# Performance work log

Hardware: AMD Instinct MI355X
Metric: run time of the kernel (lower is better)

The kernel has to match this reference:

```python
import jax, jax.numpy as jnp
import numpy as np

B, T, D = 128, 256, 1024   # batch, input_steps, input_dim
H, V, S = 1024, 1024, 128  # hidden_dim, output_dim, output_seq_length


def setup_inputs() -> dict:
    key = jax.random.key(0)
    ks = jax.random.split(key, 16)
    def w(k, shape, fan_in):
        bound = 1.0 / np.sqrt(fan_in)
        return jax.random.uniform(k, shape, jnp.float32, -bound, bound)
    return {
        "h": jax.random.normal(ks[0], (B, T, D), jnp.float32),
        # linear_h_a: Linear(D, H, bias=False); torch weight is (out, in)
        "w_h_a": w(ks[1], (H, D), D),
        # linear_s_a: Linear(H, H, bias=True)
        "w_s_a": w(ks[2], (H, H), H),
        "b_s_a": w(ks[3], (H,), H),
        # linear_a: Linear(H, 1, bias=False)
        "w_a": w(ks[4], (1, H), H),
        # linear_init_s: Linear(D, H, bias=True)
        "w_init_s": w(ks[5], (H, D), D),
        "b_init_s": w(ks[6], (H,), D),
        # GRUCell(V + D, H)
        "gru_w_ih": w(ks[7], (3 * H, V + D), H),
        "gru_w_hh": w(ks[8], (3 * H, H), H),
        "gru_b_ih": w(ks[9], (3 * H,), H),
        "gru_b_hh": w(ks[10], (3 * H,), H),
        # RNNCell(H + D, V), tanh nonlinearity
        "rnn_w_ih": w(ks[11], (V, H + D), V),
        "rnn_w_hh": w(ks[12], (V, V), V),
        "rnn_b_ih": w(ks[13], (V,), V),
        "rnn_b_hh": w(ks[14], (V,), V),
    }


def reference(h, w_h_a, w_s_a, b_s_a, w_a, w_init_s, b_init_s,
              gru_w_ih, gru_w_hh, gru_b_ih, gru_b_hh,
              rnn_w_ih, rnn_w_hh, rnn_b_ih, rnn_b_hh):
    wh = jnp.einsum('btd,hd->bth', h, w_h_a)                 # precomputed W_h @ h
    s0 = jnp.tanh(h[:, 0, :] @ w_init_s.T + b_init_s)        # (B, H)
    y0 = jnp.zeros((h.shape[0], rnn_w_ih.shape[0]), h.dtype)  # (B, V)

    def step(carry, _):
        s, y = carry
        # additive (Bahdanau) attention scores over input steps
        e = jnp.tanh(wh + (s @ w_s_a.T + b_s_a)[:, None, :])  # (B, T, H)
        scores = jnp.einsum('bth,h->bt', e, w_a[0])           # (B, T)
        a = jax.nn.softmax(scores, axis=1)
        c = jnp.einsum('bt,btd->bd', a, h)                    # context (B, D)
        # GRUCell: input = [c, y_prev], hidden = s
        x = jnp.concatenate([c, y], axis=1)
        gi = x @ gru_w_ih.T + gru_b_ih
        gh = s @ gru_w_hh.T + gru_b_hh
        ir, iz, inn = jnp.split(gi, 3, axis=1)
        hr, hz, hn = jnp.split(gh, 3, axis=1)
        r = jax.nn.sigmoid(ir + hr)
        z = jax.nn.sigmoid(iz + hz)
        n = jnp.tanh(inn + r * hn)
        s_new = (1.0 - z) * n + z * s
        # RNNCell(tanh): input = [c, s_new], hidden = y_prev; then softmax
        xr = jnp.concatenate([c, s_new], axis=1)
        pre = xr @ rnn_w_ih.T + rnn_b_ih + y @ rnn_w_hh.T + rnn_b_hh
        y_new = jax.nn.softmax(jnp.tanh(pre), axis=1)
        return (s_new, y_new), y_new

    _, ys = jax.lax.scan(step, (s0, y0), None, length=S)      # ys: (S, B, V)
    return jnp.transpose(ys, (1, 0, 2))                       # (B, S, V)
```

## Files before the change

### kernel.cpp

```cpp
#include <hip/hip_runtime.h>

typedef __bf16 bf16;
typedef __bf16 v8bf __attribute__((ext_vector_type(8)));
typedef __bf16 v4bf __attribute__((ext_vector_type(4)));
typedef float  v4f  __attribute__((ext_vector_type(4)));


static __device__ __forceinline__ float fast_tanh(float x) {
  x = fminf(fmaxf(x, -10.f), 10.f);
  float e = __expf(2.f * x);
  return (e - 1.f) * __builtin_amdgcn_rcpf(e + 1.f);
}
static __device__ __forceinline__ float fast_sigmoid(float x) {
  return __builtin_amdgcn_rcpf(1.f + __expf(-x));
}

static __device__ __forceinline__ size_t packOff(int r, int k) {
  return ((size_t)((r >> 4) * 32 + (k >> 5)) * 64 + ((k >> 3) & 3) * 16 + (r & 15)) * 8 + (k & 7);
}

template<int NKS>
static __device__ __forceinline__ void gemmTile(const bf16* __restrict__ Ap,
                                                const bf16* __restrict__ Bp,
                                                int m0, int n0, int ks0,
                                                v4f acc[2][2]) {
  const int lane = threadIdx.x & 63;
  const int w = threadIdx.x >> 6;
  const int wr = w >> 1, wc = w & 1;
  const bf16* a0p = Ap + (((size_t)((m0 >> 4) + wr * 2) * 32 + ks0) * 64 + lane) * 8;
  const bf16* b0p = Bp + (((size_t)((n0 >> 4) + wc * 2) * 32 + ks0) * 64 + lane) * 8;
#pragma unroll 8
  for (int ks = 0; ks < NKS; ks++) {
    v8bf a0 = *(const v8bf*)(a0p);
    v8bf a1 = *(const v8bf*)(a0p + 16384);
    v8bf b0 = *(const v8bf*)(b0p);
    v8bf b1 = *(const v8bf*)(b0p + 16384);
    a0p += 512; b0p += 512;
    acc[0][0] = __builtin_amdgcn_mfma_f32_16x16x32_bf16(a0, b0, acc[0][0], 0, 0, 0);
    acc[0][1] = __builtin_amdgcn_mfma_f32_16x16x32_bf16(a0, b1, acc[0][1], 0, 0, 0);
    acc[1][0] = __builtin_amdgcn_mfma_f32_16x16x32_bf16(a1, b0, acc[1][0], 0, 0, 0);
    acc[1][1] = __builtin_amdgcn_mfma_f32_16x16x32_bf16(a1, b1, acc[1][1], 0, 0, 0);
  }
}

static __device__ __forceinline__ void storeTileF32(float* __restrict__ C, int ldc,
                                                    int m0, int n0, v4f acc[2][2]) {
  const int lane = threadIdx.x & 63, w = threadIdx.x >> 6;
  const int wr = w >> 1, wc = w & 1;
  const int mB = m0 + wr * 32 + (lane >> 4) * 4;
  const int nB = n0 + wc * 32 + (lane & 15);
#pragma unroll
  for (int mf = 0; mf < 2; mf++)
#pragma unroll
    for (int nf = 0; nf < 2; nf++)
#pragma unroll
      for (int i = 0; i < 4; i++)
        C[(size_t)(mB + mf * 16 + i) * ldc + nB + nf * 16] = acc[mf][nf][i];
}

__global__ __launch_bounds__(256) void kPack(const float* __restrict__ src, int ld,
                                             bf16* __restrict__ dst, int nTh) {
  int th = blockIdx.x * 256 + threadIdx.x;
  if (th >= nTh) return;
  int rb = th >> 11, ks = (th >> 6) & 31, l = th & 63;
  int r = rb * 16 + (l & 15);
  int k = ks * 32 + ((l >> 4) & 3) * 8;
  const float* s = src + (size_t)r * ld + k;
  v4f v0 = *(const v4f*)(s);
  v4f v1 = *(const v4f*)(s + 4);
  v8bf o;
#pragma unroll
  for (int e = 0; e < 4; e++) { o[e] = (bf16)v0[e]; o[4 + e] = (bf16)v1[e]; }
  *(v8bf*)(dst + (size_t)th * 8) = o;
}

__global__ __launch_bounds__(256) void kCast4(const float* __restrict__ src,
                                              bf16* __restrict__ dst, int n4) {
  int i = blockIdx.x * 256 + threadIdx.x;
  if (i < n4) {
    v4f v = ((const v4f*)src)[i];
    ((v4bf*)dst)[i] = __builtin_convertvector(v, v4bf);
  }
}

__global__ __launch_bounds__(256) void kPrep(const float* rnn_b_ih, const float* rnn_b_hh,
                                             float* bsum, bf16* y_b16p) {
  int th = blockIdx.x * 256 + threadIdx.x;
  if (th < 16384) {
    v8bf z = {};
    ((v8bf*)y_b16p)[th] = z;
  } else {
    int j = th - 16384;
    bsum[j] = rnn_b_ih[j] + rnn_b_hh[j];
  }
}

__global__ __launch_bounds__(256) void kGemmTW(const bf16* __restrict__ Ap,
                                               const bf16* __restrict__ Bp,
                                               bf16* __restrict__ C) {
  const int nt = blockIdx.x & 15, mt = blockIdx.x >> 4;
  v4f acc[2][2] = {};
  gemmTile<32>(Ap, Bp, mt * 64, nt * 64, 0, acc);
  const int lane = threadIdx.x & 63, w = threadIdx.x >> 6;
  const int wr = w >> 1, wc = w & 1;
  const int mB = mt * 64 + wr * 32 + (lane >> 4) * 4;
  const int nB = nt * 64 + wc * 32 + (lane & 15);
#pragma unroll
  for (int mf = 0; mf < 2; mf++)
#pragma unroll
    for (int nf = 0; nf < 2; nf++)
#pragma unroll
      for (int i = 0; i < 4; i++)
        C[(size_t)(mB + mf * 16 + i) * 1024 + nB + nf * 16] = (bf16)fast_tanh(acc[mf][nf][i]);
}

__global__ __launch_bounds__(256) void kGemmS0(const bf16* __restrict__ Ap,
                                               const bf16* __restrict__ Bp,
                                               const float* __restrict__ bias,
                                               float* __restrict__ sF, bf16* __restrict__ sB) {
  const int nt = blockIdx.x & 15, mt = blockIdx.x >> 4;
  v4f acc[2][2] = {};
  gemmTile<32>(Ap, Bp, mt * 64, nt * 64, 0, acc);
  const int lane = threadIdx.x & 63, w = threadIdx.x >> 6;
  const int wr = w >> 1, wc = w & 1;
  const int mB = mt * 64 + wr * 32 + (lane >> 4) * 4;
  const int nB = nt * 64 + wc * 32 + (lane & 15);
#pragma unroll
  for (int mf = 0; mf < 2; mf++)
#pragma unroll
    for (int nf = 0; nf < 2; nf++) {
      const int n = nB + nf * 16;
      float bv = bias[n];
#pragma unroll
      for (int i = 0; i < 4; i++) {
        const int m = mB + mf * 16 + i;
        float v = fast_tanh(acc[mf][nf][i] + bv);
        size_t pi = packOff(m, n);
        sF[pi] = v;
        sB[pi] = (bf16)v;
      }
    }
}

__global__ __launch_bounds__(256) void kGemmPS(const bf16* __restrict__ Ap,
                                               const bf16* __restrict__ Bp,
                                               float* __restrict__ PS0, float* __restrict__ PS1) {
  const int t = blockIdx.x;
  const int kh = t & 1, mh = (t >> 1) & 1, nt = t >> 2;
  v4f acc[2][2] = {};
  gemmTile<16>(Ap, Bp, mh * 64, nt * 64, kh * 16, acc);
  storeTileF32(kh ? PS1 : PS0, 5120, mh * 64, nt * 64, acc);
}


static __device__ __forceinline__ void outPhase(
    int b, int step,
    const float* __restrict__ PS0, const float* __restrict__ PS1,
    const float* __restrict__ gcp0, const float* __restrict__ gcp1,
    const float* __restrict__ ygp, const float* __restrict__ bsum,
    float* __restrict__ out, bf16* __restrict__ y_b16p, float* smred) {
  const int tid = threadIdx.x, lane = tid & 63, w = tid >> 6;
  const int v0 = tid * 4;
  const size_t o5 = (size_t)b * 5120 + v0;
  const size_t o4 = (size_t)b * 4096 + 3072 + v0;
  v4f pre = *(const v4f*)(PS0 + o5);
  pre += *(const v4f*)(PS1 + o5);
  pre += *(const v4f*)(gcp0 + o4);
  pre += *(const v4f*)(gcp1 + o4);
  pre += *(const v4f*)(ygp + o4);
  pre += *(const v4f*)(bsum + v0);
  float ee[4];
  float psum = 0.f;
#pragma unroll
  for (int i = 0; i < 4; i++) { ee[i] = __expf(fast_tanh(pre[i])); psum += ee[i]; }
#pragma unroll
  for (int off = 32; off; off >>= 1) psum += __shfl_down(psum, off, 64);
  if (lane == 0) smred[w] = psum;
  __syncthreads();
  const float rden = __builtin_amdgcn_rcpf(smred[0] + smred[1] + smred[2] + smred[3]);
  v4f y4;
#pragma unroll
  for (int i = 0; i < 4; i++) y4[i] = ee[i] * rden;
  *(v4f*)(out + ((size_t)b * 128 + step) * 1024 + v0) = y4;
  *(v4bf*)(y_b16p + packOff(b, v0)) = __builtin_convertvector(y4, v4bf);
}

__global__ __launch_bounds__(256) void kScoresOut(
    const float* __restrict__ PS0, const float* __restrict__ PS1,
    const float* __restrict__ b_s_a, const float* __restrict__ w_a,
    const bf16* __restrict__ twb,
    const float* __restrict__ gcp0, const float* __restrict__ gcp1,
    const float* __restrict__ ygp, const float* __restrict__ bsum,
    float* __restrict__ esh_g, float* __restrict__ out,
    bf16* __restrict__ y_b16p, int step) {
  __shared__ float sm[2052];
  const int tid = threadIdx.x, lane = tid & 63, w = tid >> 6;
  if (blockIdx.x >= 256) {
    if (step == 0) return;
    outPhase(blockIdx.x - 256, step - 1, PS0, PS1, gcp0, gcp1, ygp, bsum,
             out, y_b16p, sm + 2048);
    return;
  }
  const int b = blockIdx.x >> 1, half = blockIdx.x & 1;
  float* ts = sm;
  float* wa = sm + 1024;
#pragma unroll
  for (int jj = 0; jj < 4; jj++) {
    int j = tid + jj * 256;
    float sa = PS0[(size_t)b * 5120 + 1024 + j] + PS1[(size_t)b * 5120 + 1024 + j] + b_s_a[j];
    float t = fast_tanh(sa);
    ts[j] = fminf(fmaxf(t, -0.99999994f), 0.99999994f);
    wa[j] = w_a[j];
  }
  __syncthreads();
  float tj[16], wj[16];
  const int h0 = lane * 16;
#pragma unroll
  for (int j = 0; j < 16; j++) { tj[j] = ts[h0 + j]; wj[j] = wa[h0 + j]; }
  const bf16* twB = twb + ((size_t)b * 256 + half * 128 + w * 32) * 1024 + h0;
  for (int ti = 0; ti < 32; ti++) {
    const bf16* p = twB + (size_t)ti * 1024;
    v8bf t8a = *(const v8bf*)p;
    v8bf t8b = *(const v8bf*)(p + 8);
    float acc = 0.f;
#pragma unroll
    for (int j = 0; j < 8; j++) {
      float tv = (float)t8a[j];
      acc += wj[j] * (tv + tj[j]) * __builtin_amdgcn_rcpf(__builtin_fmaf(tv, tj[j], 1.f));
      float tv2 = (float)t8b[j];
      acc += wj[8 + j] * (tv2 + tj[8 + j]) * __builtin_amdgcn_rcpf(__builtin_fmaf(tv2, tj[8 + j], 1.f));
    }
#pragma unroll
    for (int off = 32; off; off >>= 1) acc += __shfl_down(acc, off, 64);
    if (lane == 0) esh_g[(size_t)b * 256 + half * 128 + w * 32 + ti] = __expf(acc);
  }
}

__global__ __launch_bounds__(256) void kCtxY(
    const float* __restrict__ esh_g, const bf16* __restrict__ hb,
    const bf16* __restrict__ y_b16p, const bf16* __restrict__ W2p,
    bf16* __restrict__ c_b16p, float* __restrict__ ygp) {
  __shared__ float sm[1028];
  const int tid = threadIdx.x, lane = tid & 63, w = tid >> 6;
  if (blockIdx.x < 128) {
    const int b = blockIdx.x;
    float ev = esh_g[(size_t)b * 256 + tid];
    sm[tid] = ev;
    float p = ev;
#pragma unroll
    for (int off = 32; off; off >>= 1) p += __shfl_down(p, off, 64);
    if (lane == 0) sm[1024 + w] = p;
    __syncthreads();
    const float rden = __builtin_amdgcn_rcpf(sm[1024] + sm[1025] + sm[1026] + sm[1027]);
    const int d0 = tid * 4;
    const bf16* hp = hb + (size_t)b * 262144 + d0;
    v4f cacc = {};
#pragma unroll 8
    for (int t = 0; t < 256; t++) {
      v4bf h4 = *(const v4bf*)hp;
      hp += 1024;
      cacc += sm[t] * __builtin_convertvector(h4, v4f);
    }
    cacc *= rden;
    *(v4bf*)(c_b16p + packOff(b, d0)) = __builtin_convertvector(cacc, v4bf);
  } else {
    const int tile = blockIdx.x - 128;
    const int nt = tile & 63, mh = tile >> 6;
    v4f acc[2][2] = {};
    gemmTile<32>(y_b16p, W2p, mh * 64, nt * 64, 0, acc);
    storeTileF32(ygp, 4096, mh * 64, nt * 64, acc);
  }
}

__global__ __launch_bounds__(256) void kCGemm(
    const bf16* __restrict__ c_b16p, const bf16* __restrict__ W3p,
    float* __restrict__ gcp0, float* __restrict__ gcp1) {
  const int kh = blockIdx.x & 1, mh = (blockIdx.x >> 1) & 1, nt = blockIdx.x >> 2;
  v4f acc[2][2] = {};
  gemmTile<16>(c_b16p, W3p, mh * 64, nt * 64, kh * 16, acc);
  storeTileF32(kh ? gcp1 : gcp0, 4096, mh * 64, nt * 64, acc);
}

__global__ __launch_bounds__(256) void kGru(
    const float* __restrict__ gcp0, const float* __restrict__ gcp1,
    const float* __restrict__ ygp,
    const float* __restrict__ PS0, const float* __restrict__ PS1,
    const float* __restrict__ gru_b_ih, const float* __restrict__ gru_b_hh,
    float* __restrict__ s_f32p, bf16* __restrict__ s_b16p) {
  const int th = blockIdx.x * 256 + threadIdx.x;
  const int rb = th >> 11, ks = (th >> 6) & 31, l = th & 63;
  const int r = rb * 16 + (l & 15);
  const int j0 = ks * 32 + ((l >> 4) & 3) * 8;
  const float* g0 = gcp0 + (size_t)r * 4096 + j0;
  const float* g1 = gcp1 + (size_t)r * 4096 + j0;
  const float* yg = ygp + (size_t)r * 4096 + j0;
  const float* p0 = PS0 + (size_t)r * 5120 + j0;
  const float* p1 = PS1 + (size_t)r * 5120 + j0;
  const float* bih = gru_b_ih + j0;
  const float* bhh = gru_b_hh + j0;
  float sv[8], sn[8];
  *(v4f*)sv = *(const v4f*)(s_f32p + (size_t)th * 8);
  *(v4f*)(sv + 4) = *(const v4f*)(s_f32p + (size_t)th * 8 + 4);
#pragma unroll
  for (int e = 0; e < 8; e++) {
    float ir  = g0[e] + g1[e] + yg[e] + bih[e];
    float iz  = g0[1024 + e] + g1[1024 + e] + yg[1024 + e] + bih[1024 + e];
    float in_ = g0[2048 + e] + g1[2048 + e] + yg[2048 + e] + bih[2048 + e];
    float hr = p0[2048 + e] + p1[2048 + e] + bhh[e];
    float hz = p0[3072 + e] + p1[3072 + e] + bhh[1024 + e];
    float hn = p0[4096 + e] + p1[4096 + e] + bhh[2048 + e];
    float rg = fast_sigmoid(ir + hr);
    float zg = fast_sigmoid(iz + hz);
    float ng = fast_tanh(in_ + rg * hn);
    sn[e] = (1.f - zg) * ng + zg * sv[e];
  }
  *(v4f*)(s_f32p + (size_t)th * 8) = *(v4f*)sn;
  *(v4f*)(s_f32p + (size_t)th * 8 + 4) = *(v4f*)(sn + 4);
  v8bf sb;
#pragma unroll
  for (int e = 0; e < 8; e++) sb[e] = (bf16)sn[e];
  *(v8bf*)(s_b16p + (size_t)th * 8) = sb;
}

__global__ __launch_bounds__(256) void kOutFinal(
    const float* __restrict__ PS0, const float* __restrict__ PS1,
    const float* __restrict__ gcp0, const float* __restrict__ gcp1,
    const float* __restrict__ ygp, const float* __restrict__ bsum,
    float* __restrict__ out, bf16* __restrict__ y_b16p) {
  __shared__ float smred[4];
  outPhase(blockIdx.x, 127, PS0, PS1, gcp0, gcp1, ygp, bsum, out, y_b16p, smred);
}

extern "C" void kernel_launch(void* const* d_in, const int* in_sizes, int n_in,
                              void* d_out, int out_size, void* d_ws, size_t ws_size,
                              hipStream_t stream) {
  const float* h        = (const float*)d_in[0];
  const float* w_h_a    = (const float*)d_in[1];
  const float* w_s_a    = (const float*)d_in[2];
  const float* b_s_a    = (const float*)d_in[3];
  const float* w_a      = (const float*)d_in[4];
  const float* w_init_s = (const float*)d_in[5];
  const float* b_init_s = (const float*)d_in[6];
  const float* gru_w_ih = (const float*)d_in[7];
  const float* gru_w_hh = (const float*)d_in[8];
  const float* gru_b_ih = (const float*)d_in[9];
  const float* gru_b_hh = (const float*)d_in[10];
  const float* rnn_w_ih = (const float*)d_in[11];
  const float* rnn_w_hh = (const float*)d_in[12];
  const float* rnn_b_ih = (const float*)d_in[13];
  const float* rnn_b_hh = (const float*)d_in[14];
  (void)in_sizes; (void)n_in; (void)out_size; (void)ws_size;

  char* p = (char*)d_ws;
  auto alloc = [&](size_t bytes) { char* r = p; p += (bytes + 255) & ~(size_t)255; return r; };
  bf16* hbig   = (bf16*)alloc(33554432ull * 2);
  bf16* twb    = (bf16*)alloc(33554432ull * 2);
  bf16* h0p    = (bf16*)alloc(131072ull * 2);
  bf16* wbha_p = (bf16*)alloc(1048576ull * 2);
  bf16* wbini_p= (bf16*)alloc(1048576ull * 2);
  bf16* W2p    = (bf16*)alloc(4194304ull * 2);
  bf16* W3p    = (bf16*)alloc(4194304ull * 2);
  bf16* WP5p   = (bf16*)alloc(5242880ull * 2);
  float* PS0   = (float*)alloc(128ull * 5120 * 4);
  float* PS1   = (float*)alloc(128ull * 5120 * 4);
  float* gcp0  = (float*)alloc(128ull * 4096 * 4);
  float* gcp1  = (float*)alloc(128ull * 4096 * 4);
  float* ygp   = (float*)alloc(128ull * 4096 * 4);
  float* esh_g = (float*)alloc(128ull * 256 * 4);
  float* s_f32p= (float*)alloc(131072ull * 4);
  float* bsum  = (float*)alloc(1024ull * 4);
  bf16* s_b16p = (bf16*)alloc(131072ull * 2);
  bf16* y_b16p = (bf16*)alloc(131072ull * 2);
  bf16* c_b16p = (bf16*)alloc(131072ull * 2);
  float* out = (float*)d_out;

  kPack<<<dim3(16384), 256, 0, stream>>>(h, 1024, hbig, 4194304);
  kPack<<<dim3(64),    256, 0, stream>>>(h, 262144, h0p, 16384);
  kPack<<<dim3(512),   256, 0, stream>>>(w_h_a, 1024, wbha_p, 131072);
  kPack<<<dim3(512),   256, 0, stream>>>(w_init_s, 1024, wbini_p, 131072);
  kPack<<<dim3(1536),  256, 0, stream>>>(gru_w_ih, 2048, W3p, 393216);
  kPack<<<dim3(512),   256, 0, stream>>>(rnn_w_ih, 2048, W3p + 3145728, 131072);
  kPack<<<dim3(1536),  256, 0, stream>>>(gru_w_ih + 1024, 2048, W2p, 393216);
  kPack<<<dim3(512),   256, 0, stream>>>(rnn_w_hh, 1024, W2p + 3145728, 131072);
  kPack<<<dim3(512),   256, 0, stream>>>(rnn_w_ih + 1024, 2048, WP5p, 131072);
  kPack<<<dim3(512),   256, 0, stream>>>(w_s_a, 1024, WP5p + 1048576, 131072);
  kPack<<<dim3(1536),  256, 0, stream>>>(gru_w_hh, 1024, WP5p + 2097152, 393216);
  kPrep<<<dim3(68), 256, 0, stream>>>(rnn_b_ih, rnn_b_hh, bsum, y_b16p);

  kGemmTW<<<dim3(8192), 256, 0, stream>>>(hbig, wbha_p, twb);
  kCast4<<<dim3(32768), 256, 0, stream>>>(h, hbig, 8388608);
  kGemmS0<<<dim3(32), 256, 0, stream>>>(h0p, wbini_p, b_init_s, s_f32p, s_b16p);
  kGemmPS<<<dim3(320), 256, 0, stream>>>(s_b16p, WP5p, PS0, PS1);

  for (int step = 0; step < 128; step++) {
    kScoresOut<<<dim3(384), 256, 0, stream>>>(PS0, PS1, b_s_a, w_a, twb,
                                              gcp0, gcp1, ygp, bsum,
                                              esh_g, out, y_b16p, step);
    kCtxY<<<dim3(256), 256, 0, stream>>>(esh_g, hbig, y_b16p, W2p, c_b16p, ygp);
    kCGemm<<<dim3(256), 256, 0, stream>>>(c_b16p, W3p, gcp0, gcp1);
    kGru<<<dim3(64), 256, 0, stream>>>(gcp0, gcp1, ygp, PS0, PS1,
                                       gru_b_ih, gru_b_hh, s_f32p, s_b16p);
    kGemmPS<<<dim3(320), 256, 0, stream>>>(s_b16p, WP5p, PS0, PS1);
  }
  kOutFinal<<<dim3(128), 256, 0, stream>>>(PS0, PS1, gcp0, gcp1, ygp, bsum, out, y_b16p);
}
```

Measured before the change: 8.712 ms.

## Fuse per-step kernels into scores+context and a combined X-GEMM+GRU kernel

Cuts the per-step kernel chain from five launches to three. Attention scores and the unnormalized context are fused into one kernel, with softmax normalization deferred via partial sums. The context and y GEMMs are merged into a single concatenated-input GEMM whose epilogue applies the GRU update and emits the RNN pre-activation. The tanh-based score is also rewritten algebraically using exp(2x) precomputation, which is meant to remove per-element tanh and the extra passes through global memory. In exchange, the new exponential form risks overflow or precision loss in bf16.

```diff
diff --git a/kernel.cpp b/kernel.cpp
--- a/kernel.cpp
+++ b/kernel.cpp
@@ -15,11 +15,11 @@
   return __builtin_amdgcn_rcpf(1.f + __expf(-x));
 }
 
-static __device__ __forceinline__ size_t packOff(int r, int k) {
-  return ((size_t)((r >> 4) * 32 + (k >> 5)) * 64 + ((k >> 3) & 3) * 16 + (r & 15)) * 8 + (k & 7);
-}
-
-template<int NKS>
+static __device__ __forceinline__ size_t packOffN(int r, int k, int nksb) {
+  return ((size_t)((r >> 4) * nksb + (k >> 5)) * 64 + ((k >> 3) & 3) * 16 + (r & 15)) * 8 + (k & 7);
+}
+
+template<int NKS, int NKSB>
 static __device__ __forceinline__ void gemmTile(const bf16* __restrict__ Ap,
                                                 const bf16* __restrict__ Bp,
                                                 int m0, int n0, int ks0,
@@ -27,14 +27,14 @@
   const int lane = threadIdx.x & 63;
   const int w = threadIdx.x >> 6;
   const int wr = w >> 1, wc = w & 1;
-  const bf16* a0p = Ap + (((size_t)((m0 >> 4) + wr * 2) * 32 + ks0) * 64 + lane) * 8;
-  const bf16* b0p = Bp + (((size_t)((n0 >> 4) + wc * 2) * 32 + ks0) * 64 + lane) * 8;
+  const bf16* a0p = Ap + (((size_t)((m0 >> 4) + wr * 2) * NKSB + ks0) * 64 + lane) * 8;
+  const bf16* b0p = Bp + (((size_t)((n0 >> 4) + wc * 2) * NKSB + ks0) * 64 + lane) * 8;
 #pragma unroll 8
   for (int ks = 0; ks < NKS; ks++) {
     v8bf a0 = *(const v8bf*)(a0p);
-    v8bf a1 = *(const v8bf*)(a0p + 16384);
+    v8bf a1 = *(const v8bf*)(a0p + NKSB * 512);
     v8bf b0 = *(const v8bf*)(b0p);
-    v8bf b1 = *(const v8bf*)(b0p + 16384);
+    v8bf b1 = *(const v8bf*)(b0p + NKSB * 512);
     a0p += 512; b0p += 512;
     acc[0][0] = __builtin_amdgcn_mfma_f32_16x16x32_bf16(a0, b0, acc[0][0], 0, 0, 0);
     acc[0][1] = __builtin_amdgcn_mfma_f32_16x16x32_bf16(a0, b1, acc[0][1], 0, 0, 0);
@@ -58,8 +58,8 @@
         C[(size_t)(mB + mf * 16 + i) * ldc + nB + nf * 16] = acc[mf][nf][i];
 }
 
-__global__ __launch_bounds__(256) void kPack(const float* __restrict__ src, int ld,
-                                             bf16* __restrict__ dst, int nTh) {
+__global__ __launch_bounds__(256) void kPackG(const float* __restrict__ src, int ld,
+                                              bf16* __restrict__ dst, int nTh, int r0) {
   int th = blockIdx.x * 256 + threadIdx.x;
   if (th >= nTh) return;
   int rb = th >> 11, ks = (th >> 6) & 31, l = th & 63;
@@ -71,6 +71,30 @@
   v8bf o;
 #pragma unroll
   for (int e = 0; e < 4; e++) { o[e] = (bf16)v0[e]; o[4 + e] = (bf16)v1[e]; }
+  *(v8bf*)(dst + packOffN(r0 + r, k, 32)) = o;
+}
+
+__global__ __launch_bounds__(256) void kPackW(const float* __restrict__ gih,
+                                              const float* __restrict__ rih,
+                                              const float* __restrict__ rhh,
+                                              bf16* __restrict__ dst) {
+  const int th = blockIdx.x * 256 + threadIdx.x;
+  const int rb = th >> 12;
+  const int ks = (th >> 6) & 63;
+  const int l = th & 63;
+  const int n = rb * 16 + (l & 15);
+  const int k = ks * 32 + ((l >> 4) & 3) * 8;
+  const int g = (n >> 4) & 3;
+  const int j = ((n >> 6) << 4) | (n & 15);
+  const float* s;
+  if (g < 3)            s = gih + (size_t)(g * 1024 + j) * 2048 + k;
+  else if (k < 1024)    s = rih + (size_t)j * 2048 + k;
+  else                  s = rhh + (size_t)j * 1024 + (k - 1024);
+  v4f v0 = *(const v4f*)(s);
+  v4f v1 = *(const v4f*)(s + 4);
+  v8bf o;
+#pragma unroll
+  for (int e = 0; e < 4; e++) { o[e] = (bf16)v0[e]; o[4 + e] = (bf16)v1[e]; }
   *(v8bf*)(dst + (size_t)th * 8) = o;
 }
 
@@ -83,24 +107,38 @@
   }
 }
 
-__global__ __launch_bounds__(256) void kPrep(const float* rnn_b_ih, const float* rnn_b_hh,
-                                             float* bsum, bf16* y_b16p) {
-  int th = blockIdx.x * 256 + threadIdx.x;
-  if (th < 16384) {
+__global__ __launch_bounds__(256) void kPrep(const float* __restrict__ rnn_b_ih,
+                                             const float* __restrict__ rnn_b_hh,
+                                             const float* __restrict__ w_a,
+                                             float* __restrict__ bsum,
+                                             float* __restrict__ wsum,
+                                             bf16* __restrict__ xcatp) {
+  __shared__ float sred[4];
+  if (blockIdx.x < 64) {
+    int th = blockIdx.x * 256 + threadIdx.x;
+    int rb = th >> 11, ks = 64 + ((th >> 6) & 31), l = th & 63;
     v8bf z = {};
-    ((v8bf*)y_b16p)[th] = z;
+    *(v8bf*)(xcatp + ((size_t)(rb * 96 + ks) * 64 + l) * 8) = z;
   } else {
-    int j = th - 16384;
-    bsum[j] = rnn_b_ih[j] + rnn_b_hh[j];
-  }
-}
-
-__global__ __launch_bounds__(256) void kGemmTW(const bf16* __restrict__ Ap,
-                                               const bf16* __restrict__ Bp,
-                                               bf16* __restrict__ C) {
+    int t = threadIdx.x;
+    v4f a = *(const v4f*)(rnn_b_ih + t * 4);
+    v4f c = *(const v4f*)(rnn_b_hh + t * 4);
+    *(v4f*)(bsum + t * 4) = a + c;
+    float zz = w_a[t] + w_a[256 + t] + w_a[512 + t] + w_a[768 + t];
+#pragma unroll
+    for (int off = 32; off; off >>= 1) zz += __shfl_down(zz, off, 64);
+    if ((t & 63) == 0) sred[t >> 6] = zz;
+    __syncthreads();
+    if (t == 0) wsum[0] = sred[0] + sred[1] + sred[2] + sred[3];
+  }
+}
+
+__global__ __launch_bounds__(256) void kGemmE(const bf16* __restrict__ Ap,
+                                              const bf16* __restrict__ Bp,
+                                              bf16* __restrict__ C) {
   const int nt = blockIdx.x & 15, mt = blockIdx.x >> 4;
   v4f acc[2][2] = {};
-  gemmTile<32>(Ap, Bp, mt * 64, nt * 64, 0, acc);
+  gemmTile<32, 32>(Ap, Bp, mt * 64, nt * 64, 0, acc);
   const int lane = threadIdx.x & 63, w = threadIdx.x >> 6;
   const int wr = w >> 1, wc = w & 1;
   const int mB = mt * 64 + wr * 32 + (lane >> 4) * 4;
@@ -111,7 +149,7 @@
     for (int nf = 0; nf < 2; nf++)
 #pragma unroll
       for (int i = 0; i < 4; i++)
-        C[(size_t)(mB + mf * 16 + i) * 1024 + nB + nf * 16] = (bf16)fast_tanh(acc[mf][nf][i]);
+        C[(size_t)(mB + mf * 16 + i) * 1024 + nB + nf * 16] = (bf16)__expf(2.f * acc[mf][nf][i]);
 }
 
 __global__ __launch_bounds__(256) void kGemmS0(const bf16* __restrict__ Ap,
@@ -120,7 +158,7 @@
                                                float* __restrict__ sF, bf16* __restrict__ sB) {
   const int nt = blockIdx.x & 15, mt = blockIdx.x >> 4;
   v4f acc[2][2] = {};
-  gemmTile<32>(Ap, Bp, mt * 64, nt * 64, 0, acc);
+  gemmTile<32, 32>(Ap, Bp, mt * 64, nt * 64, 0, acc);
   const int lane = threadIdx.x & 63, w = threadIdx.x >> 6;
   const int wr = w >> 1, wc = w & 1;
   const int mB = mt * 64 + wr * 32 + (lane >> 4) * 4;
@@ -135,7 +173,7 @@
       for (int i = 0; i < 4; i++) {
         const int m = mB + mf * 16 + i;
         float v = fast_tanh(acc[mf][nf][i] + bv);
-        size_t pi = packOff(m, n);
+        size_t pi = packOffN(m, n, 32);
         sF[pi] = v;
         sB[pi] = (bf16)v;
       }
@@ -148,29 +186,25 @@
   const int t = blockIdx.x;
   const int kh = t & 1, mh = (t >> 1) & 1, nt = t >> 2;
   v4f acc[2][2] = {};
-  gemmTile<16>(Ap, Bp, mh * 64, nt * 64, kh * 16, acc);
+  gemmTile<16, 32>(Ap, Bp, mh * 64, nt * 64, kh * 16, acc);
   storeTileF32(kh ? PS1 : PS0, 5120, mh * 64, nt * 64, acc);
 }
 
 
-static __device__ __forceinline__ void outPhase(
+static __device__ __forceinline__ void outPhase256(
     int b, int step,
     const float* __restrict__ PS0, const float* __restrict__ PS1,
-    const float* __restrict__ gcp0, const float* __restrict__ gcp1,
-    const float* __restrict__ ygp, const float* __restrict__ bsum,
-    float* __restrict__ out, bf16* __restrict__ y_b16p, float* smred) {
+    const float* __restrict__ gcpR, const float* __restrict__ bsum,
+    float* __restrict__ out, bf16* __restrict__ xcatp, float* smred) {
   const int tid = threadIdx.x, lane = tid & 63, w = tid >> 6;
   const int v0 = tid * 4;
   const size_t o5 = (size_t)b * 5120 + v0;
-  const size_t o4 = (size_t)b * 4096 + 3072 + v0;
+  const size_t oR = (size_t)b * 1024 + v0;
   v4f pre = *(const v4f*)(PS0 + o5);
   pre += *(const v4f*)(PS1 + o5);
-  pre += *(const v4f*)(gcp0 + o4);
-  pre += *(const v4f*)(gcp1 + o4);
-  pre += *(const v4f*)(ygp + o4);
+  pre += *(const v4f*)(gcpR + oR);
   pre += *(const v4f*)(bsum + v0);
-  float ee[4];
-  float psum = 0.f;
+  float ee[4]; float psum = 0.f;
 #pragma unroll
   for (int i = 0; i < 4; i++) { ee[i] = __expf(fast_tanh(pre[i])); psum += ee[i]; }
 #pragma unroll
@@ -182,153 +216,171 @@
 #pragma unroll
   for (int i = 0; i < 4; i++) y4[i] = ee[i] * rden;
   *(v4f*)(out + ((size_t)b * 128 + step) * 1024 + v0) = y4;
-  *(v4bf*)(y_b16p + packOff(b, v0)) = __builtin_convertvector(y4, v4bf);
-}
-
-__global__ __launch_bounds__(256) void kScoresOut(
+  v4bf yb;
+#pragma unroll
+  for (int i = 0; i < 4; i++) yb[i] = (bf16)y4[i];
+  *(v4bf*)(xcatp + packOffN(b, 2048 + v0, 96)) = yb;
+}
+
+__global__ __launch_bounds__(256) void kFused1(
     const float* __restrict__ PS0, const float* __restrict__ PS1,
     const float* __restrict__ b_s_a, const float* __restrict__ w_a,
-    const bf16* __restrict__ twb,
-    const float* __restrict__ gcp0, const float* __restrict__ gcp1,
-    const float* __restrict__ ygp, const float* __restrict__ bsum,
-    float* __restrict__ esh_g, float* __restrict__ out,
-    bf16* __restrict__ y_b16p, int step) {
-  __shared__ float sm[2052];
+    const float* __restrict__ wsum,
+    const bf16* __restrict__ Eb, const bf16* __restrict__ hb,
+    const float* __restrict__ gcpR, const float* __restrict__ bsum,
+    float* __restrict__ Zpart, float* __restrict__ out,
+    bf16* __restrict__ xcatp, int step) {
+  __shared__ float sF[1024];
+  __shared__ float sP[128];
+  __shared__ float sred[4];
   const int tid = threadIdx.x, lane = tid & 63, w = tid >> 6;
   if (blockIdx.x >= 256) {
     if (step == 0) return;
-    outPhase(blockIdx.x - 256, step - 1, PS0, PS1, gcp0, gcp1, ygp, bsum,
-             out, y_b16p, sm + 2048);
+    outPhase256(blockIdx.x - 256, step - 1, PS0, PS1, gcpR, bsum, out, xcatp, sred);
     return;
   }
   const int b = blockIdx.x >> 1, half = blockIdx.x & 1;
-  float* ts = sm;
-  float* wa = sm + 1024;
+  {
+    const int i = tid * 4;
+    const size_t o = (size_t)b * 5120 + 1024 + i;
+    v4f sa0 = *(const v4f*)(PS0 + o);
+    v4f sa1 = *(const v4f*)(PS1 + o);
+    v4f bsa = *(const v4f*)(b_s_a + i);
+    v4f f;
+#pragma unroll
+    for (int e = 0; e < 4; e++) f[e] = __expf(2.f * (sa0[e] + sa1[e] + bsa[e]));
+    *(v4f*)&sF[i] = f;
+  }
+  __syncthreads();
+  float Fr[16], wv[16];
+  const int h0 = lane * 16;
 #pragma unroll
   for (int jj = 0; jj < 4; jj++) {
-    int j = tid + jj * 256;
-    float sa = PS0[(size_t)b * 5120 + 1024 + j] + PS1[(size_t)b * 5120 + 1024 + j] + b_s_a[j];
-    float t = fast_tanh(sa);
-    ts[j] = fminf(fmaxf(t, -0.99999994f), 0.99999994f);
-    wa[j] = w_a[j];
+    *(v4f*)&Fr[jj * 4] = *(const v4f*)&sF[h0 + jj * 4];
+    *(v4f*)&wv[jj * 4] = *(const v4f*)(w_a + h0 + jj * 4);
+  }
+  const float Wsum = wsum[0];
+  const bf16* Erow = Eb + ((size_t)b * 256 + half * 128 + w * 32) * 1024 + h0;
+  for (int ti = 0; ti < 32; ti++) {
+    v8bf ea = *(const v8bf*)(Erow);
+    v8bf eb2 = *(const v8bf*)(Erow + 8);
+    Erow += 1024;
+    float acc = 0.f;
+#pragma unroll
+    for (int jp = 0; jp < 4; jp++) {
+      float d0 = __builtin_fmaf((float)ea[2 * jp],     Fr[2 * jp],     1.f);
+      float d1 = __builtin_fmaf((float)ea[2 * jp + 1], Fr[2 * jp + 1], 1.f);
+      float nu = wv[2 * jp] * d1;
+      nu = __builtin_fmaf(wv[2 * jp + 1], d0, nu);
+      acc = __builtin_fmaf(nu, __builtin_amdgcn_rcpf(d0 * d1), acc);
+      float t0 = __builtin_fmaf((float)eb2[2 * jp],     Fr[8 + 2 * jp],     1.f);
+      float t1 = __builtin_fmaf((float)eb2[2 * jp + 1], Fr[8 + 2 * jp + 1], 1.f);
+      float nu2 = wv[8 + 2 * jp] * t1;
+      nu2 = __builtin_fmaf(wv[8 + 2 * jp + 1], t0, nu2);
+      acc = __builtin_fmaf(nu2, __builtin_amdgcn_rcpf(t0 * t1), acc);
+    }
+#pragma unroll
+    for (int off = 32; off; off >>= 1) acc += __shfl_down(acc, off, 64);
+    if (lane == 0) sP[w * 32 + ti] = __expf(Wsum - 2.f * acc);
   }
   __syncthreads();
-  float tj[16], wj[16];
-  const int h0 = lane * 16;
-#pragma unroll
-  for (int j = 0; j < 16; j++) { tj[j] = ts[h0 + j]; wj[j] = wa[h0 + j]; }
-  const bf16* twB = twb + ((size_t)b * 256 + half * 128 + w * 32) * 1024 + h0;
-  for (int ti = 0; ti < 32; ti++) {
-    const bf16* p = twB + (size_t)ti * 1024;
-    v8bf t8a = *(const v8bf*)p;
-    v8bf t8b = *(const v8bf*)(p + 8);
-    float acc = 0.f;
-#pragma unroll
-    for (int j = 0; j < 8; j++) {
-      float tv = (float)t8a[j];
-      acc += wj[j] * (tv + tj[j]) * __builtin_amdgcn_rcpf(__builtin_fmaf(tv, tj[j], 1.f));
-      float tv2 = (float)t8b[j];
-      acc += wj[8 + j] * (tv2 + tj[8 + j]) * __builtin_amdgcn_rcpf(__builtin_fmaf(tv2, tj[8 + j], 1.f));
-    }
-#pragma unroll
-    for (int off = 32; off; off >>= 1) acc += __shfl_down(acc, off, 64);
-    if (lane == 0) esh_g[(size_t)b * 256 + half * 128 + w * 32 + ti] = __expf(acc);
-  }
-}
-
-__global__ __launch_bounds__(256) void kCtxY(
-    const float* __restrict__ esh_g, const bf16* __restrict__ hb,
-    const bf16* __restrict__ y_b16p, const bf16* __restrict__ W2p,
-    bf16* __restrict__ c_b16p, float* __restrict__ ygp) {
-  __shared__ float sm[1028];
-  const int tid = threadIdx.x, lane = tid & 63, w = tid >> 6;
-  if (blockIdx.x < 128) {
-    const int b = blockIdx.x;
-    float ev = esh_g[(size_t)b * 256 + tid];
-    sm[tid] = ev;
-    float p = ev;
-#pragma unroll
-    for (int off = 32; off; off >>= 1) p += __shfl_down(p, off, 64);
-    if (lane == 0) sm[1024 + w] = p;
-    __syncthreads();
-    const float rden = __builtin_amdgcn_rcpf(sm[1024] + sm[1025] + sm[1026] + sm[1027]);
-    const int d0 = tid * 4;
-    const bf16* hp = hb + (size_t)b * 262144 + d0;
-    v4f cacc = {};
+  float zv = (tid < 128) ? sP[tid] : 0.f;
+#pragma unroll
+  for (int off = 32; off; off >>= 1) zv += __shfl_down(zv, off, 64);
+  if (lane == 0) sred[w] = zv;
+  __syncthreads();
+  if (tid == 0) Zpart[2 * b + half] = sred[0] + sred[1] + sred[2] + sred[3];
+  const int d0 = tid * 4;
+  const bf16* hp = hb + (size_t)b * 262144 + (size_t)half * 131072 + d0;
+  v4f cacc = {};
 #pragma unroll 8
-    for (int t = 0; t < 256; t++) {
-      v4bf h4 = *(const v4bf*)hp;
-      hp += 1024;
-      cacc += sm[t] * __builtin_convertvector(h4, v4f);
-    }
-    cacc *= rden;
-    *(v4bf*)(c_b16p + packOff(b, d0)) = __builtin_convertvector(cacc, v4bf);
-  } else {
-    const int tile = blockIdx.x - 128;
-    const int nt = tile & 63, mh = tile >> 6;
-    v4f acc[2][2] = {};
-    gemmTile<32>(y_b16p, W2p, mh * 64, nt * 64, 0, acc);
-    storeTileF32(ygp, 4096, mh * 64, nt * 64, acc);
-  }
-}
-
-__global__ __launch_bounds__(256) void kCGemm(
-    const bf16* __restrict__ c_b16p, const bf16* __restrict__ W3p,
-    float* __restrict__ gcp0, float* __restrict__ gcp1) {
-  const int kh = blockIdx.x & 1, mh = (blockIdx.x >> 1) & 1, nt = blockIdx.x >> 2;
-  v4f acc[2][2] = {};
-  gemmTile<16>(c_b16p, W3p, mh * 64, nt * 64, kh * 16, acc);
-  storeTileF32(kh ? gcp1 : gcp0, 4096, mh * 64, nt * 64, acc);
-}
-
-__global__ __launch_bounds__(256) void kGru(
-    const float* __restrict__ gcp0, const float* __restrict__ gcp1,
-    const float* __restrict__ ygp,
+  for (int t = 0; t < 128; t++) {
+    v4bf h4 = *(const v4bf*)hp;
+    hp += 1024;
+    cacc += sP[t] * __builtin_convertvector(h4, v4f);
+  }
+  v4bf cb;
+#pragma unroll
+  for (int e = 0; e < 4; e++) cb[e] = (bf16)cacc[e];
+  *(v4bf*)(xcatp + packOffN(b, half * 1024 + d0, 96)) = cb;
+}
+
+__global__ __launch_bounds__(768) void kXGru(
+    const bf16* __restrict__ xcatp, const bf16* __restrict__ Wbigp,
     const float* __restrict__ PS0, const float* __restrict__ PS1,
     const float* __restrict__ gru_b_ih, const float* __restrict__ gru_b_hh,
-    float* __restrict__ s_f32p, bf16* __restrict__ s_b16p) {
-  const int th = blockIdx.x * 256 + threadIdx.x;
-  const int rb = th >> 11, ks = (th >> 6) & 31, l = th & 63;
-  const int r = rb * 16 + (l & 15);
-  const int j0 = ks * 32 + ((l >> 4) & 3) * 8;
-  const float* g0 = gcp0 + (size_t)r * 4096 + j0;
-  const float* g1 = gcp1 + (size_t)r * 4096 + j0;
-  const float* yg = ygp + (size_t)r * 4096 + j0;
-  const float* p0 = PS0 + (size_t)r * 5120 + j0;
-  const float* p1 = PS1 + (size_t)r * 5120 + j0;
-  const float* bih = gru_b_ih + j0;
-  const float* bhh = gru_b_hh + j0;
-  float sv[8], sn[8];
-  *(v4f*)sv = *(const v4f*)(s_f32p + (size_t)th * 8);
-  *(v4f*)(sv + 4) = *(const v4f*)(s_f32p + (size_t)th * 8 + 4);
-#pragma unroll
-  for (int e = 0; e < 8; e++) {
-    float ir  = g0[e] + g1[e] + yg[e] + bih[e];
-    float iz  = g0[1024 + e] + g1[1024 + e] + yg[1024 + e] + bih[1024 + e];
-    float in_ = g0[2048 + e] + g1[2048 + e] + yg[2048 + e] + bih[2048 + e];
-    float hr = p0[2048 + e] + p1[2048 + e] + bhh[e];
-    float hz = p0[3072 + e] + p1[3072 + e] + bhh[1024 + e];
-    float hn = p0[4096 + e] + p1[4096 + e] + bhh[2048 + e];
-    float rg = fast_sigmoid(ir + hr);
-    float zg = fast_sigmoid(iz + hz);
+    const float* __restrict__ Zpart,
+    float* __restrict__ s_f32p, bf16* __restrict__ s_b16p,
+    float* __restrict__ gcpR) {
+  __shared__ float tl[3][64][68];
+  const int tid = threadIdx.x, lane = tid & 63, w = tid >> 6;
+  const int mh = blockIdx.x & 1, Jb = blockIdx.x >> 1;
+  const int kg = w >> 2, q = w & 3;
+  const int rb0 = mh * 4 + (q >> 1) * 2;
+  const int nb0 = Jb * 4 + (q & 1) * 2;
+  const int ksA = kg * 32;
+  const int ksB = (kg == 2) ? 32 : 0;
+  v4f acc[2][2] = {};
+  const bf16* a0p = xcatp + (((size_t)rb0 * 96 + ksA) * 64 + lane) * 8;
+  const bf16* b0p = Wbigp + (((size_t)nb0 * 64 + ksB) * 64 + lane) * 8;
+#pragma unroll 8
+  for (int ks = 0; ks < 32; ks++) {
+    v8bf a0 = *(const v8bf*)(a0p);
+    v8bf a1 = *(const v8bf*)(a0p + 96 * 512);
+    v8bf b0 = *(const v8bf*)(b0p);
+    v8bf b1 = *(const v8bf*)(b0p + 64 * 512);
+    a0p += 512; b0p += 512;
+    acc[0][0] = __builtin_amdgcn_mfma_f32_16x16x32_bf16(a0, b0, acc[0][0], 0, 0, 0);
+    acc[0][1] = __builtin_amdgcn_mfma_f32_16x16x32_bf16(a0, b1, acc[0][1], 0, 0, 0);
+    acc[1][0] = __builtin_amdgcn_mfma_f32_16x16x32_bf16(a1, b0, acc[1][0], 0, 0, 0);
+    acc[1][1] = __builtin_amdgcn_mfma_f32_16x16x32_bf16(a1, b1, acc[1][1], 0, 0, 0);
+  }
+  const int lr = (q >> 1) * 32 + ((lane >> 4) << 2);
+  const int lc = (q & 1) * 32 + (lane & 15);
+#pragma unroll
+  for (int af = 0; af < 2; af++)
+#pragma unroll
+    for (int bq = 0; bq < 2; bq++)
+#pragma unroll
+      for (int i = 0; i < 4; i++)
+        tl[kg][lr + af * 16 + i][lc + bq * 16] = acc[af][bq][i];
+  __syncthreads();
+  if (tid >= 512) return;
+  const int r = tid >> 3;
+  const int jo = (tid & 7) * 2;
+  const int row = mh * 64 + r;
+  const int jbase = Jb * 16 + jo;
+  const float rden = __builtin_amdgcn_rcpf(Zpart[2 * row] + Zpart[2 * row + 1]);
+  const size_t pb = (size_t)row * 5120;
+#pragma unroll
+  for (int u = 0; u < 2; u++) {
+    const int jj = jbase + u;
+    const int cc = jo + u;
+    float ir_ = (tl[0][r][cc]      + tl[1][r][cc])      * rden + tl[2][r][cc]      + gru_b_ih[jj];
+    float iz_ = (tl[0][r][16 + cc] + tl[1][r][16 + cc]) * rden + tl[2][r][16 + cc] + gru_b_ih[1024 + jj];
+    float in_ = (tl[0][r][32 + cc] + tl[1][r][32 + cc]) * rden + tl[2][r][32 + cc] + gru_b_ih[2048 + jj];
+    float pr_ = (tl[0][r][48 + cc] + tl[1][r][48 + cc]) * rden + tl[2][r][48 + cc];
+    float hr = PS0[pb + 2048 + jj] + PS1[pb + 2048 + jj] + gru_b_hh[jj];
+    float hz = PS0[pb + 3072 + jj] + PS1[pb + 3072 + jj] + gru_b_hh[1024 + jj];
+    float hn = PS0[pb + 4096 + jj] + PS1[pb + 4096 + jj] + gru_b_hh[2048 + jj];
+    float rg = fast_sigmoid(ir_ + hr);
+    float zg = fast_sigmoid(iz_ + hz);
     float ng = fast_tanh(in_ + rg * hn);
-    sn[e] = (1.f - zg) * ng + zg * sv[e];
-  }
-  *(v4f*)(s_f32p + (size_t)th * 8) = *(v4f*)sn;
-  *(v4f*)(s_f32p + (size_t)th * 8 + 4) = *(v4f*)(sn + 4);
-  v8bf sb;
-#pragma unroll
-  for (int e = 0; e < 8; e++) sb[e] = (bf16)sn[e];
-  *(v8bf*)(s_b16p + (size_t)th * 8) = sb;
+    size_t sp = packOffN(row, jj, 32);
+    float sv = s_f32p[sp];
+    float sn = (1.f - zg) * ng + zg * sv;
+    s_f32p[sp] = sn;
+    s_b16p[sp] = (bf16)sn;
+    gcpR[(size_t)row * 1024 + jj] = pr_;
+  }
 }
 
 __global__ __launch_bounds__(256) void kOutFinal(
     const float* __restrict__ PS0, const float* __restrict__ PS1,
-    const float* __restrict__ gcp0, const float* __restrict__ gcp1,
-    const float* __restrict__ ygp, const float* __restrict__ bsum,
-    float* __restrict__ out, bf16* __restrict__ y_b16p) {
+    const float* __restrict__ gcpR, const float* __restrict__ bsum,
+    float* __restrict__ out, bf16* __restrict__ xcatp) {
   __shared__ float smred[4];
-  outPhase(blockIdx.x, 127, PS0, PS1, gcp0, gcp1, ygp, bsum, out, y_b16p, smred);
+  outPhase256(blockIdx.x, 127, PS0, PS1, gcpR, bsum, out, xcatp, smred);
 }
 
 extern "C" void kernel_launch(void* const* d_in, const int* in_sizes, int n_in,
@@ -354,53 +406,45 @@
   char* p = (char*)d_ws;
   auto alloc = [&](size_t bytes) { char* r = p; p += (bytes + 255) & ~(size_t)255; return r; };
   bf16* hbig   = (bf16*)alloc(33554432ull * 2);
-  bf16* twb    = (bf16*)alloc(33554432ull * 2);
+  bf16* Eb     = (bf16*)alloc(33554432ull * 2);
   bf16* h0p    = (bf16*)alloc(131072ull * 2);
   bf16* wbha_p = (bf16*)alloc(1048576ull * 2);
   bf16* wbini_p= (bf16*)alloc(1048576ull * 2);
-  bf16* W2p    = (bf16*)alloc(4194304ull * 2);
-  bf16* W3p    = (bf16*)alloc(4194304ull * 2);
+  bf16* Wbigp  = (bf16*)alloc(8388608ull * 2);
   bf16* WP5p   = (bf16*)alloc(5242880ull * 2);
+  bf16* xcatp  = (bf16*)alloc(393216ull * 2);
   float* PS0   = (float*)alloc(128ull * 5120 * 4);
   float* PS1   = (float*)alloc(128ull * 5120 * 4);
-  float* gcp0  = (float*)alloc(128ull * 4096 * 4);
-  float* gcp1  = (float*)alloc(128ull * 4096 * 4);
-  float* ygp   = (float*)alloc(128ull * 4096 * 4);
-  float* esh_g = (float*)alloc(128ull * 256 * 4);
+  float* gcpR  = (float*)alloc(128ull * 1024 * 4);
   float* s_f32p= (float*)alloc(131072ull * 4);
+  bf16* s_b16p = (bf16*)alloc(131072ull * 2);
+  float* Zpart = (float*)alloc(256ull * 4);
   float* bsum  = (float*)alloc(1024ull * 4);
-  bf16* s_b16p = (bf16*)alloc(131072ull * 2);
-  bf16* y_b16p = (bf16*)alloc(131072ull * 2);
-  bf16* c_b16p = (bf16*)alloc(131072ull * 2);
+  float* wsum  = (float*)alloc(256);
   float* out = (float*)d_out;
 
-  kPack<<<dim3(16384), 256, 0, stream>>>(h, 1024, hbig, 4194304);
-  kPack<<<dim3(64),    256, 0, stream>>>(h, 262144, h0p, 16384);
-  kPack<<<dim3(512),   256, 0, stream>>>(w_h_a, 1024, wbha_p, 131072);
-  kPack<<<dim3(512),   256, 0, stream>>>(w_init_s, 1024, wbini_p, 131072);
-  kPack<<<dim3(1536),  256, 0, stream>>>(gru_w_ih, 2048, W3p, 393216);
-  kPack<<<dim3(512),   256, 0, stream>>>(rnn_w_ih, 2048, W3p + 3145728, 131072);
-  kPack<<<dim3(1536),  256, 0, stream>>>(gru_w_ih + 1024, 2048, W2p, 393216);
-  kPack<<<dim3(512),   256, 0, stream>>>(rnn_w_hh, 1024, W2p + 3145728, 131072);
-  kPack<<<dim3(512),   256, 0, stream>>>(rnn_w_ih + 1024, 2048, WP5p, 131072);
-  kPack<<<dim3(512),   256, 0, stream>>>(w_s_a, 1024, WP5p + 1048576, 131072);
-  kPack<<<dim3(1536),  256, 0, stream>>>(gru_w_hh, 1024, WP5p + 2097152, 393216);
-  kPrep<<<dim3(68), 256, 0, stream>>>(rnn_b_ih, rnn_b_hh, bsum, y_b16p);
-
-  kGemmTW<<<dim3(8192), 256, 0, stream>>>(hbig, wbha_p, twb);
+  kPackG<<<dim3(16384), 256, 0, stream>>>(h, 1024, hbig, 4194304, 0);
+  kPackG<<<dim3(64),    256, 0, stream>>>(h, 262144, h0p, 16384, 0);
+  kPackG<<<dim3(512),   256, 0, stream>>>(w_h_a, 1024, wbha_p, 131072, 0);
+  kPackG<<<dim3(512),   256, 0, stream>>>(w_init_s, 1024, wbini_p, 131072, 0);
+  kPackW<<<dim3(4096),  256, 0, stream>>>(gru_w_ih, rnn_w_ih, rnn_w_hh, Wbigp);
+  kPackG<<<dim3(512),   256, 0, stream>>>(rnn_w_ih + 1024, 2048, WP5p, 131072, 0);
+  kPackG<<<dim3(512),   256, 0, stream>>>(w_s_a, 1024, WP5p, 131072, 1024);
+  kPackG<<<dim3(1536),  256, 0, stream>>>(gru_w_hh, 1024, WP5p, 393216, 2048);
+  kPrep<<<dim3(65), 256, 0, stream>>>(rnn_b_ih, rnn_b_hh, w_a, bsum, wsum, xcatp);
+
+  kGemmE<<<dim3(8192), 256, 0, stream>>>(hbig, wbha_p, Eb);
   kCast4<<<dim3(32768), 256, 0, stream>>>(h, hbig, 8388608);
   kGemmS0<<<dim3(32), 256, 0, stream>>>(h0p, wbini_p, b_init_s, s_f32p, s_b16p);
   kGemmPS<<<dim3(320), 256, 0, stream>>>(s_b16p, WP5p, PS0, PS1);
 
   for (int step = 0; step < 128; step++) {
-    kScoresOut<<<dim3(384), 256, 0, stream>>>(PS0, PS1, b_s_a, w_a, twb,
-                                              gcp0, gcp1, ygp, bsum,
-                                              esh_g, out, y_b16p, step);
-    kCtxY<<<dim3(256), 256, 0, stream>>>(esh_g, hbig, y_b16p, W2p, c_b16p, ygp);
-    kCGemm<<<dim3(256), 256, 0, stream>>>(c_b16p, W3p, gcp0, gcp1);
-    kGru<<<dim3(64), 256, 0, stream>>>(gcp0, gcp1, ygp, PS0, PS1,
-                                       gru_b_ih, gru_b_hh, s_f32p, s_b16p);
+    kFused1<<<dim3(384), 256, 0, stream>>>(PS0, PS1, b_s_a, w_a, wsum, Eb, hbig,
+                                           gcpR, bsum, Zpart, out, xcatp, step);
+    kXGru<<<dim3(128), 768, 0, stream>>>(xcatp, Wbigp, PS0, PS1,
+                                         gru_b_ih, gru_b_hh, Zpart,
+                                         s_f32p, s_b16p, gcpR);
     kGemmPS<<<dim3(320), 256, 0, stream>>>(s_b16p, WP5p, PS0, PS1);
   }
-  kOutFinal<<<dim3(128), 256, 0, stream>>>(PS0, PS1, gcp0, gcp1, ygp, bsum, out, y_b16p);
-}
+  kOutFinal<<<dim3(128), 256, 0, stream>>>(PS0, PS1, gcpR, bsum, out, xcatp);
+}
```

New measurement: 7.960 ms. -8.6%, faster.
